# Kernel optimization log

Measured on AMD Instinct MI355X. Metric: run time of the kernel, lower is better.

## Reference

```python
import jax, jax.numpy as jnp
import numpy as np

H = 256        # hidden_size
MAX_LEN = 200  # position table has MAX_LEN+1 rows
B = 4096       # number of sessions


def setup_inputs() -> dict:
    rng = np.random.RandomState(0)
    # ragged session lengths in [10, 100)
    seq_len = rng.randint(10, 100, size=B).astype(np.int64)
    T = int(seq_len.sum())
    # reverse positions: len-1, ..., 1, 0 per session (as the torch code uses)
    reverse_pos = np.concatenate([np.arange(l - 1, -1, -1) for l in seq_len]).astype(np.int64)

    key = jax.random.key(0)
    ks = jax.random.split(key, 8)
    def lin(k, fin, fout):
        # torch Linear init ~ U(-1/sqrt(fin), 1/sqrt(fin)); store as [fin, fout]
        lim = 1.0 / np.sqrt(fin)
        kw, kb = jax.random.split(k)
        W = jax.random.uniform(kw, (fin, fout), jnp.float32, -lim, lim)
        b = jax.random.uniform(kb, (fout,), jnp.float32, -lim, lim)
        return W, b

    hidden = jax.random.normal(ks[0], (T, H), jnp.float32)
    pos_table = jax.random.normal(ks[1], (MAX_LEN + 1, H), jnp.float32)
    W_pos, b_pos = lin(ks[2], 2 * H, H)   # W_pos_inter
    W1, b1 = lin(ks[3], H, H)             # W_1_inter
    W2, b2 = lin(ks[4], H, H)             # W_2_inter
    qw, qb = lin(ks[5], H, 1)             # q_inter

    return {
        "hidden": hidden,
        "pos_table": pos_table,
        "W_pos": W_pos, "b_pos": b_pos,
        "W1": W1, "b1": b1,
        "W2": W2, "b2": b2,
        "qw": qw, "qb": qb,
        "seq_len": jnp.asarray(seq_len),
        "reverse_pos": jnp.asarray(reverse_pos),
    }


def reference(hidden, pos_table, W_pos, b_pos, W1, b1, W2, b2, qw, qb, seq_len, reverse_pos):
    T = hidden.shape[0]
    nb = seq_len.shape[0]
    # segment id per token (sessions are contiguous)
    seg = jnp.repeat(jnp.arange(nb), seq_len, total_repeat_length=T)  # [T]
    # per-session mean, gathered back per token (v_mean_repeat_concat)
    sess_mean = jax.ops.segment_sum(hidden, seg, num_segments=nb)
    sess_mean = sess_mean / seq_len[:, None].astype(hidden.dtype)
    v_mean = sess_mean[seg]                                           # [T, H]
    # position-augmented hidden: tanh(W_pos_inter([hidden; pos_emb]))
    pos_emb = pos_table[reverse_pos]                                  # [T, H]
    pos_hidden = jnp.tanh(jnp.concatenate([hidden, pos_emb], -1) @ W_pos + b_pos)
    # alpha = q_inter(sigmoid(W_1_inter(v_mean) + W_2_inter(pos_hidden)))
    gate = jax.nn.sigmoid(v_mean @ W1 + b1 + pos_hidden @ W2 + b2)
    alpha = gate @ qw + qb                                            # [T, 1]
    # per-session weighted sum of hidden
    h_s = jax.ops.segment_sum(alpha * hidden, seg, num_segments=nb)   # [B, H]
    return h_s
```

## Files before the change

kernel.cpp:

```cpp
#include <hip/hip_runtime.h>
#include <hip/hip_bf16.h>
#include <stdint.h>

#define HD 256
#define BM 64
#define APAD 8
#define ASTRIDE (HD + APAD)

typedef __bf16 bf16x8 __attribute__((ext_vector_type(8)));
typedef float f32x4 __attribute__((ext_vector_type(4)));
typedef unsigned short ushort8v __attribute__((ext_vector_type(8)));
typedef unsigned short us4 __attribute__((ext_vector_type(4)));

__device__ __forceinline__ unsigned short f2bf(float f) {
    unsigned int x = __float_as_uint(f);
    unsigned int r = (x + 0x7FFFu + ((x >> 16) & 1u)) >> 16;
    return (unsigned short)r;
}

__global__ void scan_kernel(const int* __restrict__ seq_len, int* __restrict__ offsets, int B) {
    __shared__ int sums[256];
    int tid = threadIdx.x;
    int per = (B + 255) / 256;
    int b0 = tid * per;
    int local[32];
    int tot = 0;
    for (int i = 0; i < per && i < 32; ++i) {
        int b = b0 + i;
        int v = (b < B) ? seq_len[b] : 0;
        local[i] = tot;
        tot += v;
    }
    sums[tid] = tot;
    __syncthreads();
    for (int off = 1; off < 256; off <<= 1) {
        int v = (tid >= off) ? sums[tid - off] : 0;
        __syncthreads();
        sums[tid] += v;
        __syncthreads();
    }
    int start = sums[tid] - tot;
    for (int i = 0; i < per && i < 32; ++i) {
        int b = b0 + i;
        if (b < B) offsets[b] = start + local[i];
    }
    if (tid == 255) offsets[B] = sums[255];
}

__global__ void mean_kernel(const float* __restrict__ hidden, const int* __restrict__ offsets,
                            unsigned short* __restrict__ mean_bf, unsigned short* __restrict__ hb,
                            int* __restrict__ seg) {
    int b = blockIdx.x;
    int s = offsets[b], e = offsets[b + 1];
    int tid = threadIdx.x;
    for (int t = s + tid; t < e; t += 256) seg[t] = b;
    int g = tid >> 6, c = tid & 63;
    float4 acc = {0.f, 0.f, 0.f, 0.f};
    for (int t = s + g; t < e; t += 4) {
        const float4 v = *reinterpret_cast<const float4*>(hidden + (size_t)t * HD + c * 4);
        acc.x += v.x; acc.y += v.y; acc.z += v.z; acc.w += v.w;
        if (hb) {
            us4 pk;
            pk[0] = f2bf(v.x); pk[1] = f2bf(v.y); pk[2] = f2bf(v.z); pk[3] = f2bf(v.w);
            *reinterpret_cast<us4*>(hb + (size_t)t * HD + c * 4) = pk;
        }
    }
    __shared__ float4 part[4][64];
    part[g][c] = acc;
    __syncthreads();
    if (g == 0) {
        float4 a0 = part[0][c], a1 = part[1][c], a2 = part[2][c], a3 = part[3][c];
        float inv = 1.0f / (float)(e - s);
        us4 pk;
        pk[0] = f2bf((a0.x + a1.x + a2.x + a3.x) * inv);
        pk[1] = f2bf((a0.y + a1.y + a2.y + a3.y) * inv);
        pk[2] = f2bf((a0.z + a1.z + a2.z + a3.z) * inv);
        pk[3] = f2bf((a0.w + a1.w + a2.w + a3.w) * inv);
        *reinterpret_cast<us4*>(mean_bf + (size_t)b * HD + c * 4) = pk;
    }
}

__global__ void transpose_kernel(const float* __restrict__ Wp, const float* __restrict__ W1,
                                 const float* __restrict__ W2,
                                 unsigned short* __restrict__ WphT, unsigned short* __restrict__ WpbT,
                                 unsigned short* __restrict__ W1T, unsigned short* __restrict__ W2T) {
    int n = blockIdx.x;
    int k = threadIdx.x;
    WphT[n * HD + k] = f2bf(Wp[k * HD + n]);
    WpbT[n * HD + k] = f2bf(Wp[(HD + k) * HD + n]);
    W1T[n * HD + k]  = f2bf(W1[k * HD + n]);
    W2T[n * HD + k]  = f2bf(W2[k * HD + n]);
}

__global__ __launch_bounds__(256) void small_gemm_kernel(
    const unsigned short* __restrict__ mean_bf, int Mu, int nbu,
    const float* __restrict__ pos_table, int Mp,
    const unsigned short* __restrict__ W1T, const unsigned short* __restrict__ WpbT,
    const float* __restrict__ b1, const float* __restrict__ b2, const float* __restrict__ bp,
    float* __restrict__ u, float* __restrict__ P2) {
    __shared__ __align__(16) unsigned short As[16][ASTRIDE];
    int tid = threadIdx.x;
    bool isU = (int)blockIdx.x < nbu;
    int m0 = isU ? blockIdx.x * 16 : (blockIdx.x - nbu) * 16;
    int M  = isU ? Mu : Mp;
    const unsigned short* BT = isU ? W1T : WpbT;
    float* out = isU ? u : P2;

    {
        int row = tid >> 4;
        int colg = (tid & 15) * 16;
        int m = m0 + row;
        if (isU) {
            ushort8v v0 = {0,0,0,0,0,0,0,0}, v1 = {0,0,0,0,0,0,0,0};
            if (m < M) {
                v0 = *reinterpret_cast<const ushort8v*>(mean_bf + (size_t)m * HD + colg);
                v1 = *reinterpret_cast<const ushort8v*>(mean_bf + (size_t)m * HD + colg + 8);
            }
            *reinterpret_cast<ushort8v*>(&As[row][colg])     = v0;
            *reinterpret_cast<ushort8v*>(&As[row][colg + 8]) = v1;
        } else {
            float4 f[4] = {{0,0,0,0},{0,0,0,0},{0,0,0,0},{0,0,0,0}};
            if (m < M) {
                const float4* p = reinterpret_cast<const float4*>(pos_table + (size_t)m * HD + colg);
                f[0] = p[0]; f[1] = p[1]; f[2] = p[2]; f[3] = p[3];
            }
            ushort8v v0, v1;
            v0[0]=f2bf(f[0].x); v0[1]=f2bf(f[0].y); v0[2]=f2bf(f[0].z); v0[3]=f2bf(f[0].w);
            v0[4]=f2bf(f[1].x); v0[5]=f2bf(f[1].y); v0[6]=f2bf(f[1].z); v0[7]=f2bf(f[1].w);
            v1[0]=f2bf(f[2].x); v1[1]=f2bf(f[2].y); v1[2]=f2bf(f[2].z); v1[3]=f2bf(f[2].w);
            v1[4]=f2bf(f[3].x); v1[5]=f2bf(f[3].y); v1[6]=f2bf(f[3].z); v1[7]=f2bf(f[3].w);
            *reinterpret_cast<ushort8v*>(&As[row][colg])     = v0;
            *reinterpret_cast<ushort8v*>(&As[row][colg + 8]) = v1;
        }
    }
    __syncthreads();

    int wave = tid >> 6, lane = tid & 63, quad = lane >> 4, cc = lane & 15;
    int nb = wave * 64;
    f32x4 acc4[4];
    for (int i = 0; i < 4; ++i) acc4[i] = (f32x4){0.f, 0.f, 0.f, 0.f};

    bf16x8 wfp[4];
    for (int nf = 0; nf < 4; ++nf)
        wfp[nf] = *reinterpret_cast<const bf16x8*>(BT + (size_t)(nb + nf * 16 + cc) * HD + quad * 8);
    for (int kc8 = 0; kc8 < 8; ++kc8) {
        int kc = kc8 * 32;
        bf16x8 wfc[4];
        for (int nf = 0; nf < 4; ++nf) wfc[nf] = wfp[nf];
        if (kc8 < 7)
            for (int nf = 0; nf < 4; ++nf)
                wfp[nf] = *reinterpret_cast<const bf16x8*>(BT + (size_t)(nb + nf * 16 + cc) * HD + kc + 32 + quad * 8);
        bf16x8 af = *reinterpret_cast<const bf16x8*>(&As[cc][kc + quad * 8]);
        for (int nf = 0; nf < 4; ++nf)
            acc4[nf] = __builtin_amdgcn_mfma_f32_16x16x32_bf16(af, wfc[nf], acc4[nf], 0, 0, 0);
    }
    for (int nf = 0; nf < 4; ++nf)
        for (int r = 0; r < 4; ++r) {
            int row = m0 + quad * 4 + r;
            int col = nb + nf * 16 + cc;
            if (row < M) {
                float bias = isU ? (b1[col] + b2[col]) : bp[col];
                out[(size_t)row * HD + col] = acc4[nf][r] + bias;
            }
        }
}

__global__ __launch_bounds__(256, 3) void main_kernel(
    const float* __restrict__ hidden, const unsigned short* __restrict__ hb, int T,
    const unsigned short* __restrict__ WphT,
    const unsigned short* __restrict__ W2T,
    const float* __restrict__ P2,
    const float* __restrict__ u,
    const float* __restrict__ qw, const float* __restrict__ qb,
    const int* __restrict__ rp, const int* __restrict__ seg,
    float* __restrict__ alpha) {
    __shared__ __align__(16) unsigned short Ah[BM][ASTRIDE];
    __shared__ int rp_s[BM];
    __shared__ int seg_s[BM];
    __shared__ float alpha_s[BM];

    int tid = threadIdx.x;
    int t0 = blockIdx.x * BM;
    int wave = tid >> 6, lane = tid & 63, quad = lane >> 4, cc = lane & 15;
    int mb = wave * 64;

    bf16x8 afp[4];
    for (int mf = 0; mf < 4; ++mf)
        afp[mf] = *reinterpret_cast<const bf16x8*>(WphT + (size_t)(mb + mf * 16 + cc) * HD + quad * 8);

    {
        int row = tid >> 2;
        int t = t0 + row;
        if (hb) {
            for (int i = 0; i < 8; ++i) {
                int cg = (tid & 3) * 8 + 32 * i;
                ushort8v v = {0,0,0,0,0,0,0,0};
                if (t < T) v = *reinterpret_cast<const ushort8v*>(hb + (size_t)t * HD + cg);
                *reinterpret_cast<ushort8v*>(&Ah[row][cg]) = v;
            }
        } else {
            for (int i = 0; i < 8; ++i) {
                int cg = (tid & 3) * 8 + 32 * i;
                float4 f0 = {0,0,0,0}, f1 = {0,0,0,0};
                if (t < T) {
                    const float4* p = reinterpret_cast<const float4*>(hidden + (size_t)t * HD + cg);
                    f0 = p[0]; f1 = p[1];
                }
                ushort8v pk;
                pk[0] = f2bf(f0.x); pk[1] = f2bf(f0.y); pk[2] = f2bf(f0.z); pk[3] = f2bf(f0.w);
                pk[4] = f2bf(f1.x); pk[5] = f2bf(f1.y); pk[6] = f2bf(f1.z); pk[7] = f2bf(f1.w);
                *reinterpret_cast<ushort8v*>(&Ah[row][cg]) = pk;
            }
        }
    }
    if (tid < BM) {
        int t = t0 + tid;
        rp_s[tid]  = (t < T) ? rp[t] : 0;
        seg_s[tid] = (t < T) ? seg[t] : 0;
        alpha_s[tid] = qb[0];
    }
    __syncthreads();

    f32x4 acc[4][4];
    for (int i = 0; i < 4; ++i) for (int j = 0; j < 4; ++j) acc[i][j] = (f32x4){0.f, 0.f, 0.f, 0.f};

    for (int kc8 = 0; kc8 < 8; ++kc8) {
        int kc = kc8 * 32;
        bf16x8 afc[4];
        for (int mf = 0; mf < 4; ++mf) afc[mf] = afp[mf];
        if (kc8 < 7)
            for (int mf = 0; mf < 4; ++mf)
                afp[mf] = *reinterpret_cast<const bf16x8*>(WphT + (size_t)(mb + mf * 16 + cc) * HD + kc + 32 + quad * 8);
        bf16x8 bfr[4];
        for (int nf = 0; nf < 4; ++nf)
            bfr[nf] = *reinterpret_cast<const bf16x8*>(&Ah[nf * 16 + cc][kc + quad * 8]);
        for (int mf = 0; mf < 4; ++mf)
            for (int nf = 0; nf < 4; ++nf)
                acc[mf][nf] = __builtin_amdgcn_mfma_f32_16x16x32_bf16(afc[mf], bfr[nf], acc[mf][nf], 0, 0, 0);
    }
    __syncthreads();

    bf16x8 wfp[4];
    for (int nf = 0; nf < 4; ++nf)
        wfp[nf] = *reinterpret_cast<const bf16x8*>(W2T + (size_t)(mb + nf * 16 + cc) * HD + quad * 8);

    for (int mf = 0; mf < 4; ++mf)
        for (int nf = 0; nf < 4; ++nf) {
            int token = nf * 16 + cc;
            int h0 = mb + mf * 16 + quad * 4;
            const float4 p2v = *reinterpret_cast<const float4*>(P2 + (size_t)rp_s[token] * HD + h0);
            us4 pk;
            {
                float v0 = acc[mf][nf][0] + p2v.x;
                float v1 = acc[mf][nf][1] + p2v.y;
                float v2 = acc[mf][nf][2] + p2v.z;
                float v3 = acc[mf][nf][3] + p2v.w;
                float e0 = __expf(2.f * v0), e1 = __expf(2.f * v1);
                float e2 = __expf(2.f * v2), e3 = __expf(2.f * v3);
                pk[0] = f2bf(1.f - 2.f / (e0 + 1.f));
                pk[1] = f2bf(1.f - 2.f / (e1 + 1.f));
                pk[2] = f2bf(1.f - 2.f / (e2 + 1.f));
                pk[3] = f2bf(1.f - 2.f / (e3 + 1.f));
            }
            *reinterpret_cast<us4*>(&Ah[token][h0]) = pk;
            acc[mf][nf] = (f32x4){0.f, 0.f, 0.f, 0.f};
        }
    __syncthreads();

    for (int kc8 = 0; kc8 < 8; ++kc8) {
        int kc = kc8 * 32;
        bf16x8 wfc[4];
        for (int nf = 0; nf < 4; ++nf) wfc[nf] = wfp[nf];
        if (kc8 < 7)
            for (int nf = 0; nf < 4; ++nf)
                wfp[nf] = *reinterpret_cast<const bf16x8*>(W2T + (size_t)(mb + nf * 16 + cc) * HD + kc + 32 + quad * 8);
        for (int mf = 0; mf < 4; ++mf) {
            bf16x8 af = *reinterpret_cast<const bf16x8*>(&Ah[mf * 16 + cc][kc + quad * 8]);
            for (int nf = 0; nf < 4; ++nf)
                acc[mf][nf] = __builtin_amdgcn_mfma_f32_16x16x32_bf16(af, wfc[nf], acc[mf][nf], 0, 0, 0);
        }
    }

    float qwv[4];
    for (int nf = 0; nf < 4; ++nf) qwv[nf] = qw[mb + nf * 16 + cc];
    for (int mf = 0; mf < 4; ++mf)
        for (int r = 0; r < 4; ++r) {
            int token = mf * 16 + quad * 4 + r;
            const float* urow = u + (size_t)seg_s[token] * HD;
            float s = 0.f;
            for (int nf = 0; nf < 4; ++nf) {
                float g = acc[mf][nf][r] + urow[mb + nf * 16 + cc];
                g = 1.0f / (1.0f + __expf(-g));
                s += g * qwv[nf];
            }
            s += __shfl_xor(s, 1);
            s += __shfl_xor(s, 2);
            s += __shfl_xor(s, 4);
            s += __shfl_xor(s, 8);
            if (cc == 0) atomicAdd(&alpha_s[token], s);
        }
    __syncthreads();
    if (tid < BM) {
        int t = t0 + tid;
        if (t < T) alpha[t] = alpha_s[tid];
    }
}

__global__ void hs_kernel(const float* __restrict__ hidden, const unsigned short* __restrict__ hb,
                          const float* __restrict__ alpha,
                          const int* __restrict__ offsets, float* __restrict__ out) {
    int b = blockIdx.x;
    int s = offsets[b], e = offsets[b + 1];
    int tid = threadIdx.x;
    __shared__ float al[256];
    for (int i = tid; i < e - s; i += 256) al[i] = alpha[s + i];
    __syncthreads();
    int g = tid >> 6, c = tid & 63;
    float4 acc = {0.f, 0.f, 0.f, 0.f};
    if (hb) {
        for (int t = s + g; t < e; t += 4) {
            float a = al[t - s];
            us4 v = *reinterpret_cast<const us4*>(hb + (size_t)t * HD + c * 4);
            acc.x += a * __uint_as_float(((unsigned)v[0]) << 16);
            acc.y += a * __uint_as_float(((unsigned)v[1]) << 16);
            acc.z += a * __uint_as_float(((unsigned)v[2]) << 16);
            acc.w += a * __uint_as_float(((unsigned)v[3]) << 16);
        }
    } else {
        for (int t = s + g; t < e; t += 4) {
            float a = al[t - s];
            const float4 v = *reinterpret_cast<const float4*>(hidden + (size_t)t * HD + c * 4);
            acc.x += a * v.x; acc.y += a * v.y; acc.z += a * v.z; acc.w += a * v.w;
        }
    }
    __shared__ float4 part[4][64];
    part[g][c] = acc;
    __syncthreads();
    if (g == 0) {
        float4 a0 = part[0][c], a1 = part[1][c], a2 = part[2][c], a3 = part[3][c];
        float4 m;
        m.x = a0.x + a1.x + a2.x + a3.x;
        m.y = a0.y + a1.y + a2.y + a3.y;
        m.z = a0.z + a1.z + a2.z + a3.z;
        m.w = a0.w + a1.w + a2.w + a3.w;
        *reinterpret_cast<float4*>(out + (size_t)b * HD + c * 4) = m;
    }
}

extern "C" void kernel_launch(void* const* d_in, const int* in_sizes, int n_in,
                              void* d_out, int out_size, void* d_ws, size_t ws_size,
                              hipStream_t stream) {
    (void)n_in; (void)out_size;
    const float* hidden    = (const float*)d_in[0];
    const float* pos_table = (const float*)d_in[1];
    const float* W_pos     = (const float*)d_in[2];
    const float* b_pos     = (const float*)d_in[3];
    const float* W1        = (const float*)d_in[4];
    const float* b1        = (const float*)d_in[5];
    const float* W2        = (const float*)d_in[6];
    const float* b2        = (const float*)d_in[7];
    const float* qw        = (const float*)d_in[8];
    const float* qb        = (const float*)d_in[9];
    const int* seq_len     = (const int*)d_in[10];
    const int* reverse_pos = (const int*)d_in[11];

    int T  = in_sizes[0] / HD;
    int B  = in_sizes[10];
    int NP = in_sizes[1] / HD;

    char* ws = (char*)d_ws;
    char* ws_end = ws + ws_size;
    auto carve = [&](size_t bytes) -> char* {
        char* p = ws;
        ws += (bytes + 255) & ~(size_t)255;
        return p;
    };
    int* offsets          = (int*)carve((size_t)(B + 1) * sizeof(int));
    int* seg              = (int*)carve((size_t)T * sizeof(int));
    unsigned short* meanb = (unsigned short*)carve((size_t)B * HD * 2);
    float* u              = (float*)carve((size_t)B * HD * sizeof(float));
    float* P2             = (float*)carve((size_t)NP * HD * sizeof(float));
    unsigned short* WphT  = (unsigned short*)carve((size_t)HD * HD * 2);
    unsigned short* WpbT  = (unsigned short*)carve((size_t)HD * HD * 2);
    unsigned short* W1T   = (unsigned short*)carve((size_t)HD * HD * 2);
    unsigned short* W2T   = (unsigned short*)carve((size_t)HD * HD * 2);
    float* alpha          = (float*)carve((size_t)T * sizeof(float));
    unsigned short* hb    = nullptr;
    if ((size_t)(ws_end - ws) >= (size_t)T * HD * 2 + 256)
        hb = (unsigned short*)carve((size_t)T * HD * 2);

    int nbu = (B + 15) / 16;
    int nbp = (NP + 15) / 16;

    scan_kernel<<<1, 256, 0, stream>>>(seq_len, offsets, B);
    transpose_kernel<<<HD, HD, 0, stream>>>(W_pos, W1, W2, WphT, WpbT, W1T, W2T);
    mean_kernel<<<B, 256, 0, stream>>>(hidden, offsets, meanb, hb, seg);
    small_gemm_kernel<<<nbu + nbp, 256, 0, stream>>>(meanb, B, nbu, pos_table, NP,
                                                     W1T, WpbT, b1, b2, b_pos, u, P2);
    main_kernel<<<(T + BM - 1) / BM, 256, 0, stream>>>(hidden, hb, T, WphT, W2T, P2, u, qw, qb,
                                                       reverse_pos, seg, alpha);
    hs_kernel<<<B, 256, 0, stream>>>(hidden, hb, alpha, offsets, (float*)d_out);
}
```

Before: 575.3 us.

## Fuse session weighted-sum into main kernel with atomic accumulation, transpose second GEMM

Removes the separate hs_kernel and alpha buffer: each main_kernel block now computes its 64 tokens' alpha values, then scans them per column and atomically adds the per-session partial sums into a zeroed output. A new zero_kernel clears the output first. The second GEMM swaps operand roles so each lane holds four contiguous hidden units, which allows float4 loads of u and qw and a cheaper cross-lane reduction; loops are also explicitly unrolled. In exchange it adds global float atomics, which makes the summation order nondeterministic, and a column loop that runs serially over the block's rows.

```diff
diff --git a/kernel.cpp b/kernel.cpp
--- a/kernel.cpp
+++ b/kernel.cpp
@@ -16,6 +16,11 @@
     unsigned int x = __float_as_uint(f);
     unsigned int r = (x + 0x7FFFu + ((x >> 16) & 1u)) >> 16;
     return (unsigned short)r;
+}
+
+__global__ void zero_kernel(float4* __restrict__ p, int n) {
+    int i = blockIdx.x * blockDim.x + threadIdx.x;
+    if (i < n) p[i] = make_float4(0.f, 0.f, 0.f, 0.f);
 }
 
 __global__ void scan_kernel(const int* __restrict__ seq_len, int* __restrict__ offsets, int B) {
@@ -173,7 +178,7 @@
     const float* __restrict__ u,
     const float* __restrict__ qw, const float* __restrict__ qb,
     const int* __restrict__ rp, const int* __restrict__ seg,
-    float* __restrict__ alpha) {
+    float* __restrict__ out) {
     __shared__ __align__(16) unsigned short Ah[BM][ASTRIDE];
     __shared__ int rp_s[BM];
     __shared__ int seg_s[BM];
@@ -185,6 +190,7 @@
     int mb = wave * 64;
 
     bf16x8 afp[4];
+    #pragma unroll
     for (int mf = 0; mf < 4; ++mf)
         afp[mf] = *reinterpret_cast<const bf16x8*>(WphT + (size_t)(mb + mf * 16 + cc) * HD + quad * 8);
 
@@ -192,6 +198,7 @@
         int row = tid >> 2;
         int t = t0 + row;
         if (hb) {
+            #pragma unroll
             for (int i = 0; i < 8; ++i) {
                 int cg = (tid & 3) * 8 + 32 * i;
                 ushort8v v = {0,0,0,0,0,0,0,0};
@@ -199,6 +206,7 @@
                 *reinterpret_cast<ushort8v*>(&Ah[row][cg]) = v;
             }
         } else {
+            #pragma unroll
             for (int i = 0; i < 8; ++i) {
                 int cg = (tid & 3) * 8 + 32 * i;
                 float4 f0 = {0,0,0,0}, f1 = {0,0,0,0};
@@ -222,33 +230,45 @@
     __syncthreads();
 
     f32x4 acc[4][4];
-    for (int i = 0; i < 4; ++i) for (int j = 0; j < 4; ++j) acc[i][j] = (f32x4){0.f, 0.f, 0.f, 0.f};
+    #pragma unroll
+    for (int i = 0; i < 4; ++i)
+        #pragma unroll
+        for (int j = 0; j < 4; ++j) acc[i][j] = (f32x4){0.f, 0.f, 0.f, 0.f};
 
     for (int kc8 = 0; kc8 < 8; ++kc8) {
         int kc = kc8 * 32;
         bf16x8 afc[4];
+        #pragma unroll
         for (int mf = 0; mf < 4; ++mf) afc[mf] = afp[mf];
         if (kc8 < 7)
+            #pragma unroll
             for (int mf = 0; mf < 4; ++mf)
                 afp[mf] = *reinterpret_cast<const bf16x8*>(WphT + (size_t)(mb + mf * 16 + cc) * HD + kc + 32 + quad * 8);
         bf16x8 bfr[4];
+        #pragma unroll
         for (int nf = 0; nf < 4; ++nf)
             bfr[nf] = *reinterpret_cast<const bf16x8*>(&Ah[nf * 16 + cc][kc + quad * 8]);
+        #pragma unroll
         for (int mf = 0; mf < 4; ++mf)
+            #pragma unroll
             for (int nf = 0; nf < 4; ++nf)
                 acc[mf][nf] = __builtin_amdgcn_mfma_f32_16x16x32_bf16(afc[mf], bfr[nf], acc[mf][nf], 0, 0, 0);
     }
     __syncthreads();
 
     bf16x8 wfp[4];
-    for (int nf = 0; nf < 4; ++nf)
-        wfp[nf] = *reinterpret_cast<const bf16x8*>(W2T + (size_t)(mb + nf * 16 + cc) * HD + quad * 8);
-
+    #pragma unroll
     for (int mf = 0; mf < 4; ++mf)
-        for (int nf = 0; nf < 4; ++nf) {
-            int token = nf * 16 + cc;
+        wfp[mf] = *reinterpret_cast<const bf16x8*>(W2T + (size_t)(mb + mf * 16 + cc) * HD + quad * 8);
+
+    #pragma unroll
+    for (int nf = 0; nf < 4; ++nf) {
+        int token = nf * 16 + cc;
+        const float* p2row = P2 + (size_t)rp_s[token] * HD;
+        #pragma unroll
+        for (int mf = 0; mf < 4; ++mf) {
             int h0 = mb + mf * 16 + quad * 4;
-            const float4 p2v = *reinterpret_cast<const float4*>(P2 + (size_t)rp_s[token] * HD + h0);
+            const float4 p2v = *reinterpret_cast<const float4*>(p2row + h0);
             us4 pk;
             {
                 float v0 = acc[mf][nf][0] + p2v.x;
@@ -265,85 +285,73 @@
             *reinterpret_cast<us4*>(&Ah[token][h0]) = pk;
             acc[mf][nf] = (f32x4){0.f, 0.f, 0.f, 0.f};
         }
+    }
     __syncthreads();
 
     for (int kc8 = 0; kc8 < 8; ++kc8) {
         int kc = kc8 * 32;
         bf16x8 wfc[4];
-        for (int nf = 0; nf < 4; ++nf) wfc[nf] = wfp[nf];
+        #pragma unroll
+        for (int mf = 0; mf < 4; ++mf) wfc[mf] = wfp[mf];
         if (kc8 < 7)
-            for (int nf = 0; nf < 4; ++nf)
-                wfp[nf] = *reinterpret_cast<const bf16x8*>(W2T + (size_t)(mb + nf * 16 + cc) * HD + kc + 32 + quad * 8);
+            #pragma unroll
+            for (int mf = 0; mf < 4; ++mf)
+                wfp[mf] = *reinterpret_cast<const bf16x8*>(W2T + (size_t)(mb + mf * 16 + cc) * HD + kc + 32 + quad * 8);
+        #pragma unroll
+        for (int nf = 0; nf < 4; ++nf) {
+            bf16x8 af = *reinterpret_cast<const bf16x8*>(&Ah[nf * 16 + cc][kc + quad * 8]);
+            #pragma unroll
+            for (int mf = 0; mf < 4; ++mf)
+                acc[mf][nf] = __builtin_amdgcn_mfma_f32_16x16x32_bf16(wfc[mf], af, acc[mf][nf], 0, 0, 0);
+        }
+    }
+
+    float4 qv[4];
+    #pragma unroll
+    for (int mf = 0; mf < 4; ++mf)
+        qv[mf] = *reinterpret_cast<const float4*>(qw + mb + mf * 16 + quad * 4);
+    #pragma unroll
+    for (int nf = 0; nf < 4; ++nf) {
+        int token = nf * 16 + cc;
+        const float* urow = u + (size_t)seg_s[token] * HD;
+        float s = 0.f;
+        #pragma unroll
         for (int mf = 0; mf < 4; ++mf) {
-            bf16x8 af = *reinterpret_cast<const bf16x8*>(&Ah[mf * 16 + cc][kc + quad * 8]);
-            for (int nf = 0; nf < 4; ++nf)
-                acc[mf][nf] = __builtin_amdgcn_mfma_f32_16x16x32_bf16(af, wfc[nf], acc[mf][nf], 0, 0, 0);
-        }
-    }
-
-    float qwv[4];
-    for (int nf = 0; nf < 4; ++nf) qwv[nf] = qw[mb + nf * 16 + cc];
-    for (int mf = 0; mf < 4; ++mf)
-        for (int r = 0; r < 4; ++r) {
-            int token = mf * 16 + quad * 4 + r;
-            const float* urow = u + (size_t)seg_s[token] * HD;
-            float s = 0.f;
-            for (int nf = 0; nf < 4; ++nf) {
-                float g = acc[mf][nf][r] + urow[mb + nf * 16 + cc];
+            int n0 = mb + mf * 16 + quad * 4;
+            const float4 uv = *reinterpret_cast<const float4*>(urow + n0);
+            #pragma unroll
+            for (int r = 0; r < 4; ++r) {
+                float g = acc[mf][nf][r] + ((const float*)&uv)[r];
                 g = 1.0f / (1.0f + __expf(-g));
-                s += g * qwv[nf];
-            }
-            s += __shfl_xor(s, 1);
-            s += __shfl_xor(s, 2);
-            s += __shfl_xor(s, 4);
-            s += __shfl_xor(s, 8);
-            if (cc == 0) atomicAdd(&alpha_s[token], s);
-        }
-    __syncthreads();
-    if (tid < BM) {
-        int t = t0 + tid;
-        if (t < T) alpha[t] = alpha_s[tid];
-    }
-}
-
-__global__ void hs_kernel(const float* __restrict__ hidden, const unsigned short* __restrict__ hb,
-                          const float* __restrict__ alpha,
-                          const int* __restrict__ offsets, float* __restrict__ out) {
-    int b = blockIdx.x;
-    int s = offsets[b], e = offsets[b + 1];
-    int tid = threadIdx.x;
-    __shared__ float al[256];
-    for (int i = tid; i < e - s; i += 256) al[i] = alpha[s + i];
-    __syncthreads();
-    int g = tid >> 6, c = tid & 63;
-    float4 acc = {0.f, 0.f, 0.f, 0.f};
-    if (hb) {
-        for (int t = s + g; t < e; t += 4) {
-            float a = al[t - s];
-            us4 v = *reinterpret_cast<const us4*>(hb + (size_t)t * HD + c * 4);
-            acc.x += a * __uint_as_float(((unsigned)v[0]) << 16);
-            acc.y += a * __uint_as_float(((unsigned)v[1]) << 16);
-            acc.z += a * __uint_as_float(((unsigned)v[2]) << 16);
-            acc.w += a * __uint_as_float(((unsigned)v[3]) << 16);
-        }
-    } else {
-        for (int t = s + g; t < e; t += 4) {
-            float a = al[t - s];
-            const float4 v = *reinterpret_cast<const float4*>(hidden + (size_t)t * HD + c * 4);
-            acc.x += a * v.x; acc.y += a * v.y; acc.z += a * v.z; acc.w += a * v.w;
-        }
-    }
-    __shared__ float4 part[4][64];
-    part[g][c] = acc;
-    __syncthreads();
-    if (g == 0) {
-        float4 a0 = part[0][c], a1 = part[1][c], a2 = part[2][c], a3 = part[3][c];
-        float4 m;
-        m.x = a0.x + a1.x + a2.x + a3.x;
-        m.y = a0.y + a1.y + a2.y + a3.y;
-        m.z = a0.z + a1.z + a2.z + a3.z;
-        m.w = a0.w + a1.w + a2.w + a3.w;
-        *reinterpret_cast<float4*>(out + (size_t)b * HD + c * 4) = m;
+                s += g * ((const float*)&qv[mf])[r];
+            }
+        }
+        s += __shfl_xor(s, 16);
+        s += __shfl_xor(s, 32);
+        if (quad == 0) atomicAdd(&alpha_s[token], s);
+    }
+    __syncthreads();
+
+    {
+        int col = tid;
+        int nrows = T - t0; if (nrows > BM) nrows = BM;
+        float accv = 0.f;
+        int curb = seg_s[0];
+        if (hb) {
+            for (int i = 0; i < nrows; ++i) {
+                int b = seg_s[i];
+                if (b != curb) { atomicAdd(out + (size_t)curb * HD + col, accv); accv = 0.f; curb = b; }
+                unsigned short hv = hb[(size_t)(t0 + i) * HD + col];
+                accv += alpha_s[i] * __uint_as_float(((unsigned)hv) << 16);
+            }
+        } else {
+            for (int i = 0; i < nrows; ++i) {
+                int b = seg_s[i];
+                if (b != curb) { atomicAdd(out + (size_t)curb * HD + col, accv); accv = 0.f; curb = b; }
+                accv += alpha_s[i] * hidden[(size_t)(t0 + i) * HD + col];
+            }
+        }
+        atomicAdd(out + (size_t)curb * HD + col, accv);
     }
 }
 
@@ -384,20 +392,20 @@
     unsigned short* WpbT  = (unsigned short*)carve((size_t)HD * HD * 2);
     unsigned short* W1T   = (unsigned short*)carve((size_t)HD * HD * 2);
     unsigned short* W2T   = (unsigned short*)carve((size_t)HD * HD * 2);
-    float* alpha          = (float*)carve((size_t)T * sizeof(float));
     unsigned short* hb    = nullptr;
     if ((size_t)(ws_end - ws) >= (size_t)T * HD * 2 + 256)
         hb = (unsigned short*)carve((size_t)T * HD * 2);
 
     int nbu = (B + 15) / 16;
     int nbp = (NP + 15) / 16;
-
+    int nout4 = (B * HD) / 4;
+
+    zero_kernel<<<(nout4 + 255) / 256, 256, 0, stream>>>((float4*)d_out, nout4);
     scan_kernel<<<1, 256, 0, stream>>>(seq_len, offsets, B);
     transpose_kernel<<<HD, HD, 0, stream>>>(W_pos, W1, W2, WphT, WpbT, W1T, W2T);
     mean_kernel<<<B, 256, 0, stream>>>(hidden, offsets, meanb, hb, seg);
     small_gemm_kernel<<<nbu + nbp, 256, 0, stream>>>(meanb, B, nbu, pos_table, NP,
                                                      W1T, WpbT, b1, b2, b_pos, u, P2);
     main_kernel<<<(T + BM - 1) / BM, 256, 0, stream>>>(hidden, hb, T, WphT, W2T, P2, u, qw, qb,
-                                                       reverse_pos, seg, alpha);
-    hs_kernel<<<B, 256, 0, stream>>>(hidden, hb, alpha, offsets, (float*)d_out);
-}
+                                                       reverse_pos, seg, (float*)d_out);
+}
```

Measured after the change: 612.9 us. +6.5%, slower.
